# Optimization experiments

Measured on AMD Instinct MI355X. Metric: run time of the kernel, lower is better.

Reference implementation:

```python
import jax, jax.numpy as jnp
import numpy as np

GROUP = 16  # FP4 quantization group size along the K (channel) axis
FP4_MAX = 6.0  # max magnitude representable in e2m1


def _round_e2m1(v):
    """Round to nearest value on the signed e2m1 grid {0,.5,1,1.5,2,3,4,6}."""
    s = jnp.sign(v)
    a = jnp.clip(jnp.abs(v), 0.0, FP4_MAX)
    q = jnp.where(a < 0.25, 0.0,
        jnp.where(a < 0.75, 0.5,
        jnp.where(a < 1.25, 1.0,
        jnp.where(a < 1.75, 1.5,
        jnp.where(a < 2.5, 2.0,
        jnp.where(a < 3.5, 3.0,
        jnp.where(a < 5.0, 4.0, 6.0)))))))
    return s * q


def fake_quant_fp4(x):
    """NVFP4-style fake quantization: per-16 group fp8_e4m3 scale + e2m1 values.

    x: [..., K] with K % 16 == 0. Returns dequantized tensor, same shape/dtype.
    """
    shp = x.shape
    g = x.reshape(shp[:-1] + (shp[-1] // GROUP, GROUP))
    amax = jnp.max(jnp.abs(g), axis=-1, keepdims=True)
    # scale stored as fp8_e4m3 (matches oscales dtype float8_e4m3fn in source)
    scale = (amax / FP4_MAX).astype(jnp.float8_e4m3fn).astype(x.dtype)
    safe = jnp.where(scale > 0, scale, jnp.ones_like(scale))
    q = _round_e2m1(g / safe)
    dq = jnp.where(scale > 0, q * scale, jnp.zeros_like(q))
    return dq.reshape(shp)


def setup_inputs() -> dict:
    key = jax.random.key(0)
    k1, k2, k3 = jax.random.split(key, 3)
    M, K, N = 8192, 4096, 4096
    x = jax.random.normal(k1, (M, K), dtype=jnp.float32)
    weight = jax.random.normal(k2, (N, K), dtype=jnp.float32) * 0.02
    bias = jax.random.normal(k3, (N,), dtype=jnp.float32) * 0.01
    return {"x": x, "weight": weight, "bias": bias}


def reference(x, weight, bias):
    # quantize_input: per-group FP4 fake-quant of activations (smooth == ones)
    xq = fake_quant_fp4(x)
    # __init__ quantizes weight_pad with the same kernel -> qweight/wscales
    wq = fake_quant_fp4(weight)
    # gemm_w4a4 with inline dequant + bias add
    out = jnp.einsum("mk,nk->mn", xq, wq) + bias
    return out
```

## Files before the change

kernel.cpp:

```cpp
#include <hip/hip_runtime.h>
#include <cstdint>


typedef __attribute__((ext_vector_type(8))) __bf16 bf16x8;
typedef __attribute__((ext_vector_type(16))) float f32x16;

typedef __attribute__((address_space(1))) void gvoid;
typedef __attribute__((address_space(3))) void lvoid;

__device__ __forceinline__ float fp8_e4m3_rt(float x) {
    if (x < 0.015625f) {
        return __builtin_rintf(x * 512.0f) * (1.0f / 512.0f);
    }
    unsigned u = __float_as_uint(x);
    unsigned lsb = (u >> 20) & 1u;
    u = (u + 0x7FFFFu + lsb) & ~0xFFFFFu;
    return __uint_as_float(u);
}

__device__ __forceinline__ uint2 quant_quad(float4 v) {
    float ax = fabsf(v.x), ay = fabsf(v.y), az = fabsf(v.z), aw = fabsf(v.w);
    float a = fmaxf(fmaxf(ax, ay), fmaxf(az, aw));
    a = fmaxf(a, __shfl_xor(a, 1));
    a = fmaxf(a, __shfl_xor(a, 2));
    float scale = fp8_e4m3_rt(a / 6.0f);
    float sN = -scale;
    float n0 = sN * 0x1p-27f;
    float n1 = sN * 0x1p-25f;
    float n2 = sN * 0x1p-24f;
    float n4 = sN * 0x1p-23f;
    float n6 = sN * 0x1p-22f;
    float e[4] = {v.x, v.y, v.z, v.w};
    unsigned r[4];
    #pragma unroll
    for (int i = 0; i < 4; ++i) {
        float av = fabsf(e[i]);
        float q =
            fmaf(sN, 0.25f, av) < n0 ? 0.0f :
            fmaf(sN, 0.75f, av) < n1 ? 0.5f :
            fmaf(sN, 1.25f, av) < n2 ? 1.0f :
            fmaf(sN, 1.75f, av) < n2 ? 1.5f :
            fmaf(sN, 2.5f,  av) < n4 ? 2.0f :
            fmaf(sN, 3.5f,  av) < n4 ? 3.0f :
            fmaf(sN, 5.0f,  av) < n6 ? 4.0f : 6.0f;
        float dq = q * scale;
        r[i] = (__float_as_uint(dq) | (__float_as_uint(e[i]) & 0x80000000u)) >> 16;
    }
    uint2 o;
    o.x = r[0] | (r[1] << 16);
    o.y = r[2] | (r[3] << 16);
    return o;
}

__global__ __launch_bounds__(256)
void quant_fp4_fused(const float* __restrict__ x, const float* __restrict__ w,
                     uint16_t* __restrict__ out, int xquads, int totquads) {
    const int half = totquads >> 1;
    const int t0 = blockIdx.x * 256 + threadIdx.x;
    uint2* o2 = (uint2*)out;
    if (t0 < half) {
        const float4* s0 = (t0 < xquads) ? ((const float4*)x) + t0
                                         : ((const float4*)w) + (t0 - xquads);
        o2[t0] = quant_quad(*s0);
    }
    const int q1 = t0 + half;
    if (q1 < totquads) {
        const float4* s1 = (q1 < xquads) ? ((const float4*)x) + q1
                                         : ((const float4*)w) + (q1 - xquads);
        o2[q1] = quant_quad(*s1);
    }
}

#define BM 256
#define BN 256
#define BK 64
#define THREADS 512

#define STG_A(bb, i, kk)                                                     \
    __builtin_amdgcn_global_load_lds((gvoid*)(Aq + (size_t)offA[i] + (kk)),  \
        (lvoid*)&lds[bb][0][ldsU + (i) * 4096], 16, 0, 0)
#define STG_B(bb, i, kk)                                                     \
    __builtin_amdgcn_global_load_lds((gvoid*)(Bq + (size_t)offB[i] + (kk)),  \
        (lvoid*)&lds[bb][1][ldsU + (i) * 4096], 16, 0, 0)

__global__ __launch_bounds__(THREADS, 2)
void gemm_w4a4(const uint16_t* __restrict__ Aq, const uint16_t* __restrict__ Bq,
               const float* __restrict__ bias, float* __restrict__ C,
               int M, int N, int K) {
    __shared__ __align__(16) uint16_t lds[2][2][BM * BK];

    const int tid  = threadIdx.x;
    const int wave = tid >> 6;
    const int lane = tid & 63;
    const int wm   = wave >> 2;
    const int wn   = wave & 3;
    const int l31  = lane & 31;
    const int hi8  = (lane >> 5) << 3;
    const int rsw  = (lane & 7) << 3;

    int kx[4];
    #pragma unroll
    for (int ks = 0; ks < 4; ++ks) kx[ks] = (ks * 16 + hi8) ^ rsw;

    const int aRow = ((wm << 7) + l31) << 6;
    const int bRow = ((wn << 6) + l31) << 6;
    const int ldsU = wave << 9;

    const int ntm = M >> 8, ntn = N >> 8, nwg = ntm * ntn;
    const int bid = blockIdx.x;
    const int q8 = nwg >> 3, r8 = nwg & 7;
    const int xcd = bid & 7;
    const int wgid = (xcd < r8 ? xcd * (q8 + 1) : r8 * (q8 + 1) + (xcd - r8) * q8)
                     + (bid >> 3);
    const int mBase = (wgid % ntm) << 8;
    const int nBase = (wgid / ntm) << 8;
    (void)ntn;

    uint32_t offA[4], offB[4];
    #pragma unroll
    for (int i = 0; i < 4; ++i) {
        const int c   = i * THREADS + tid;
        const int row = c >> 3;
        const int kc  = ((c & 7) ^ (row & 7)) << 3;
        offA[i] = (uint32_t)(mBase + row) * (uint32_t)K + (uint32_t)kc;
        offB[i] = (uint32_t)(nBase + row) * (uint32_t)K + (uint32_t)kc;
    }

    const int nt = K / BK;

    #pragma unroll
    for (int i = 0; i < 4; ++i) STG_A(0, i, 0);
    #pragma unroll
    for (int i = 0; i < 4; ++i) STG_B(0, i, 0);

    f32x16 acc[4][2] = {};

    for (int tk = 0; tk < nt; ++tk) {
        const int bb = tk & 1;
        const uint16_t* lA = &lds[bb][0][0];
        const uint16_t* lB = &lds[bb][1][0];

        asm volatile("" ::: "memory");
        __builtin_amdgcn_s_barrier();
        asm volatile("" ::: "memory");

        if (tk + 1 < nt) {
            const int kk = (tk + 1) * BK;
            #pragma unroll
            for (int i = 0; i < 4; ++i) STG_A(bb ^ 1, i, kk);
            #pragma unroll
            for (int i = 0; i < 4; ++i) STG_B(bb ^ 1, i, kk);
            asm volatile("s_waitcnt vmcnt(8)" ::: "memory");
        } else {
            asm volatile("s_waitcnt vmcnt(0)" ::: "memory");
        }
        __builtin_amdgcn_s_barrier();
        asm volatile("" ::: "memory");

        bf16x8 aC[4], bC[2], aN[4], bN[2];
        #pragma unroll
        for (int mi = 0; mi < 4; ++mi)
            aC[mi] = *(const bf16x8*)&lA[aRow + mi * 2048 + kx[0]];
        #pragma unroll
        for (int ni = 0; ni < 2; ++ni)
            bC[ni] = *(const bf16x8*)&lB[bRow + ni * 2048 + kx[0]];

        #pragma unroll
        for (int ks = 0; ks < 4; ++ks) {
            if (ks < 3) {
                #pragma unroll
                for (int mi = 0; mi < 4; ++mi)
                    aN[mi] = *(const bf16x8*)&lA[aRow + mi * 2048 + kx[ks + 1]];
                #pragma unroll
                for (int ni = 0; ni < 2; ++ni)
                    bN[ni] = *(const bf16x8*)&lB[bRow + ni * 2048 + kx[ks + 1]];
            }
            __builtin_amdgcn_s_setprio(1);
            #pragma unroll
            for (int mi = 0; mi < 4; ++mi)
                #pragma unroll
                for (int ni = 0; ni < 2; ++ni)
                    acc[mi][ni] = __builtin_amdgcn_mfma_f32_32x32x16_bf16(
                        aC[mi], bC[ni], acc[mi][ni], 0, 0, 0);
            __builtin_amdgcn_s_setprio(0);
            if (ks < 3) {
                #pragma unroll
                for (int mi = 0; mi < 4; ++mi) aC[mi] = aN[mi];
                #pragma unroll
                for (int ni = 0; ni < 2; ++ni) bC[ni] = bN[ni];
            }
        }
    }

    #pragma unroll
    for (int ni = 0; ni < 2; ++ni) {
        const int col = nBase + (wn << 6) + ni * 32 + l31;
        const float bj = bias[col];
        #pragma unroll
        for (int mi = 0; mi < 4; ++mi) {
            const int rowb = mBase + (wm << 7) + mi * 32 + ((lane >> 5) << 2);
            #pragma unroll
            for (int r = 0; r < 16; ++r) {
                const int row = rowb + (r & 3) + ((r >> 2) << 3);
                C[(size_t)row * N + col] = acc[mi][ni][r] + bj;
            }
        }
    }
}

extern "C" void kernel_launch(void* const* d_in, const int* in_sizes, int n_in,
                              void* d_out, int out_size, void* d_ws, size_t ws_size,
                              hipStream_t stream) {
    const float* x    = (const float*)d_in[0];
    const float* w    = (const float*)d_in[1];
    const float* bias = (const float*)d_in[2];
    float* out = (float*)d_out;

    const int N = in_sizes[2];
    const int K = in_sizes[1] / N;
    const int M = in_sizes[0] / K;

    uint16_t* xq = (uint16_t*)d_ws;
    uint16_t* wq = xq + (size_t)M * K;
    (void)wq;

    const int xquads = (M * K) / 4;
    const int totquads = xquads + (N * K) / 4;
    const int half = totquads / 2;
    quant_fp4_fused<<<(half + 255) / 256, 256, 0, stream>>>(x, w, xq, xquads, totquads);

    const int nwg = (M >> 8) * (N >> 8);
    gemm_w4a4<<<nwg, THREADS, 0, stream>>>(xq, wq, bias, out, M, N, K);
}
```

Before: 520.8 us.

## Restructure GEMM mainloop into four-phase pipelined schedule with 16x16x32 MFMA

After: 702.5 us. 1.35x slower.

```diff
diff --git a/kernel.cpp b/kernel.cpp
--- a/kernel.cpp
+++ b/kernel.cpp
@@ -3,7 +3,7 @@
 
 
 typedef __attribute__((ext_vector_type(8))) __bf16 bf16x8;
-typedef __attribute__((ext_vector_type(16))) float f32x16;
+typedef __attribute__((ext_vector_type(4))) float f32x4;
 
 typedef __attribute__((address_space(1))) void gvoid;
 typedef __attribute__((address_space(3))) void lvoid;
@@ -71,42 +71,104 @@
     }
 }
 
-#define BM 256
-#define BN 256
 #define BK 64
 #define THREADS 512
 
-#define STG_A(bb, i, kk)                                                     \
-    __builtin_amdgcn_global_load_lds((gvoid*)(Aq + (size_t)offA[i] + (kk)),  \
-        (lvoid*)&lds[bb][0][ldsU + (i) * 4096], 16, 0, 0)
-#define STG_B(bb, i, kk)                                                     \
-    __builtin_amdgcn_global_load_lds((gvoid*)(Bq + (size_t)offB[i] + (kk)),  \
-        (lvoid*)&lds[bb][1][ldsU + (i) * 4096], 16, 0, 0)
+#define SB __builtin_amdgcn_sched_barrier(0)
+
+#define LDA(dst, B_, mh) do { _Pragma("unroll")                               \
+    for (int fi_ = 0; fi_ < 4; ++fi_) {                                       \
+        dst[fi_][0] = *(const bf16x8*)&lds[B_][0][aRowA + (mh)*4096 + fi_*1024 + kx0]; \
+        dst[fi_][1] = *(const bf16x8*)&lds[B_][0][aRowA + (mh)*4096 + fi_*1024 + kx1]; \
+    } } while (0)
+
+#define LDB(dst, B_, nh) do { _Pragma("unroll")                               \
+    for (int fj_ = 0; fj_ < 2; ++fj_) {                                       \
+        dst[fj_][0] = *(const bf16x8*)&lds[B_][1][bRowB + (nh)*8192 + fj_*1024 + kx0]; \
+        dst[fj_][1] = *(const bf16x8*)&lds[B_][1][bRowB + (nh)*8192 + fj_*1024 + kx1]; \
+    } } while (0)
+
+#define STGA(B_, ch, ko) __builtin_amdgcn_global_load_lds(                    \
+    (gvoid*)(pA + offA[ch] + kAdv + (ko)),                                    \
+    (lvoid*)&lds[B_][0][(ch)*4096 + ldsU], 16, 0, 0)
+#define STGB(B_, ch, ko) __builtin_amdgcn_global_load_lds(                    \
+    (gvoid*)(pB + offB[ch] + kAdv + (ko)),                                    \
+    (lvoid*)&lds[B_][1][(ch)*4096 + ldsU], 16, 0, 0)
+
+#define QUAD(A_, Bf_, mh, nh) do {                                            \
+    __builtin_amdgcn_s_setprio(1);                                            \
+    _Pragma("unroll") for (int fi_ = 0; fi_ < 4; ++fi_)                       \
+    _Pragma("unroll") for (int fj_ = 0; fj_ < 2; ++fj_) {                     \
+        f32x4 c_ = acc[(mh)*4 + fi_][(nh)*2 + fj_];                           \
+        c_ = __builtin_amdgcn_mfma_f32_16x16x32_bf16(A_[fi_][0], Bf_[fj_][0], c_, 0, 0, 0); \
+        c_ = __builtin_amdgcn_mfma_f32_16x16x32_bf16(A_[fi_][1], Bf_[fj_][1], c_, 0, 0, 0); \
+        acc[(mh)*4 + fi_][(nh)*2 + fj_] = c_;                                 \
+    }                                                                         \
+    __builtin_amdgcn_s_setprio(0); } while (0)
+
+#define PHEND do { SB; __builtin_amdgcn_s_barrier(); SB; } while (0)
+
+#define KTILE(B_, STG_, AHD_, SK_) do {                                       \
+                                                                     \
+    LDB(b1, B_, 1);                                                           \
+    if (STG_) { STGA(B_, 0, SK_); STGA(B_, 2, SK_); }                         \
+    asm volatile("s_waitcnt lgkmcnt(4)" ::: "memory");                        \
+    if (STG_) { asm volatile("s_waitcnt vmcnt(10)" ::: "memory"); }           \
+    else      { asm volatile("s_waitcnt vmcnt(0)"  ::: "memory"); }           \
+    SB; __builtin_amdgcn_s_barrier(); SB;                                     \
+    QUAD(a0, b0, 0, 0);                                                       \
+    PHEND;                                                                    \
+                                                                     \
+    LDA(a1, B_, 1);                                                           \
+    if (STG_) { STGB(B_, 0, SK_); STGB(B_, 1, SK_); }                         \
+    asm volatile("s_waitcnt lgkmcnt(8)" ::: "memory");                        \
+    if (STG_) { asm volatile("s_waitcnt vmcnt(10)" ::: "memory"); }           \
+    SB; __builtin_amdgcn_s_barrier(); SB;                                     \
+    QUAD(a0, b1, 0, 1);                                                       \
+    PHEND;                                                                    \
+                                                                     \
+    if (AHD_) { LDA(a0, (B_) ^ 1, 0); }                                       \
+    if (STG_) { STGB(B_, 2, SK_); STGB(B_, 3, SK_); }                         \
+    if (AHD_) { asm volatile("s_waitcnt lgkmcnt(8)" ::: "memory"); }          \
+    else      { asm volatile("s_waitcnt lgkmcnt(0)" ::: "memory"); }          \
+    if (STG_) { asm volatile("s_waitcnt vmcnt(10)" ::: "memory"); }           \
+    SB; __builtin_amdgcn_s_barrier(); SB;                                     \
+    QUAD(a1, b1, 1, 1);                                                       \
+    PHEND;                                                                    \
+                                                                     \
+    if (AHD_) { LDB(nb0, (B_) ^ 1, 0); }                                      \
+    if (STG_) { STGA(B_, 1, SK_); STGA(B_, 3, SK_); }                         \
+    if (AHD_) { asm volatile("s_waitcnt lgkmcnt(4)" ::: "memory"); }          \
+    else      { asm volatile("s_waitcnt lgkmcnt(0)" ::: "memory"); }          \
+    if (STG_) { asm volatile("s_waitcnt vmcnt(10)" ::: "memory"); }           \
+    SB; __builtin_amdgcn_s_barrier(); SB;                                     \
+    QUAD(a1, b0, 1, 0);                                                       \
+    if (AHD_) { _Pragma("unroll") for (int z_ = 0; z_ < 2; ++z_) {            \
+        b0[z_][0] = nb0[z_][0]; b0[z_][1] = nb0[z_][1]; } }                   \
+    PHEND;                                                                    \
+    } while (0)
 
 __global__ __launch_bounds__(THREADS, 2)
 void gemm_w4a4(const uint16_t* __restrict__ Aq, const uint16_t* __restrict__ Bq,
                const float* __restrict__ bias, float* __restrict__ C,
                int M, int N, int K) {
-    __shared__ __align__(16) uint16_t lds[2][2][BM * BK];
+    __shared__ __align__(16) uint16_t lds[2][2][256 * BK];
 
     const int tid  = threadIdx.x;
     const int wave = tid >> 6;
     const int lane = tid & 63;
     const int wm   = wave >> 2;
     const int wn   = wave & 3;
-    const int l31  = lane & 31;
-    const int hi8  = (lane >> 5) << 3;
+    const int l15  = lane & 15;
+    const int hi16 = (lane >> 4) << 3;
     const int rsw  = (lane & 7) << 3;
-
-    int kx[4];
-    #pragma unroll
-    for (int ks = 0; ks < 4; ++ks) kx[ks] = (ks * 16 + hi8) ^ rsw;
-
-    const int aRow = ((wm << 7) + l31) << 6;
-    const int bRow = ((wn << 6) + l31) << 6;
-    const int ldsU = wave << 9;
-
-    const int ntm = M >> 8, ntn = N >> 8, nwg = ntm * ntn;
+    const int kx0  = hi16 ^ rsw;
+    const int kx1  = (32 + hi16) ^ rsw;
+    const int aRowA = ((wm << 7) + l15) << 6;
+    const int bRowB = ((wn << 5) + l15) << 6;
+    const int ldsU  = wave << 9;
+
+    const int ntm = M >> 8, nwg = ntm * (N >> 8);
     const int bid = blockIdx.x;
     const int q8 = nwg >> 3, r8 = nwg & 7;
     const int xcd = bid & 7;
@@ -114,96 +176,59 @@
                      + (bid >> 3);
     const int mBase = (wgid % ntm) << 8;
     const int nBase = (wgid / ntm) << 8;
-    (void)ntn;
 
     uint32_t offA[4], offB[4];
     #pragma unroll
     for (int i = 0; i < 4; ++i) {
-        const int c   = i * THREADS + tid;
-        const int row = c >> 3;
-        const int kc  = ((c & 7) ^ (row & 7)) << 3;
-        offA[i] = (uint32_t)(mBase + row) * (uint32_t)K + (uint32_t)kc;
-        offB[i] = (uint32_t)(nBase + row) * (uint32_t)K + (uint32_t)kc;
-    }
+        const int c = i * THREADS + tid;
+        const int p = c >> 3;
+        const int kc = ((c & 7) ^ (p & 7)) << 3;
+        offA[i] = (uint32_t)p * (uint32_t)K + (uint32_t)kc;
+        const int nh = p >> 7, wnn = (p >> 5) & 3, r = p & 31;
+        const int Lr = wnn * 64 + nh * 32 + r;
+        offB[i] = (uint32_t)Lr * (uint32_t)K + (uint32_t)kc;
+    }
+    const uint16_t* pA = Aq + (size_t)mBase * K;
+    const uint16_t* pB = Bq + (size_t)nBase * K;
 
     const int nt = K / BK;
 
+    uint32_t kAdv = 0;
+
+    STGA(0, 0, 0); STGA(0, 2, 0); STGB(0, 0, 0); STGB(0, 1, 0);
+    STGB(0, 2, 0); STGB(0, 3, 0); STGA(0, 1, 0); STGA(0, 3, 0);
+    STGA(1, 0, 64); STGA(1, 2, 64); STGB(1, 0, 64); STGB(1, 1, 64);
+    STGB(1, 2, 64); STGB(1, 3, 64); STGA(1, 1, 64); STGA(1, 3, 64);
+    asm volatile("s_waitcnt vmcnt(8)" ::: "memory");
+    SB; __builtin_amdgcn_s_barrier(); SB;
+
+    f32x4 acc[8][4] = {};
+    bf16x8 a0[4][2], a1[4][2], b0[2][2], b1[2][2], nb0[2][2];
+
+    LDA(a0, 0, 0);
+    LDB(b0, 0, 0);
+
+    kAdv = 2 * BK;
+
+    for (int tk = 0; tk < nt - 2; tk += 2) {
+        KTILE(0, 1, 1, 0);
+        KTILE(1, 1, 1, 64);
+        kAdv += 2 * BK;
+    }
+    KTILE(0, 0, 1, 0);
+    KTILE(1, 0, 0, 0);
+
+    const int rq = (lane >> 4) << 2;
     #pragma unroll
-    for (int i = 0; i < 4; ++i) STG_A(0, i, 0);
-    #pragma unroll
-    for (int i = 0; i < 4; ++i) STG_B(0, i, 0);
-
-    f32x16 acc[4][2] = {};
-
-    for (int tk = 0; tk < nt; ++tk) {
-        const int bb = tk & 1;
-        const uint16_t* lA = &lds[bb][0][0];
-        const uint16_t* lB = &lds[bb][1][0];
-
-        asm volatile("" ::: "memory");
-        __builtin_amdgcn_s_barrier();
-        asm volatile("" ::: "memory");
-
-        if (tk + 1 < nt) {
-            const int kk = (tk + 1) * BK;
-            #pragma unroll
-            for (int i = 0; i < 4; ++i) STG_A(bb ^ 1, i, kk);
-            #pragma unroll
-            for (int i = 0; i < 4; ++i) STG_B(bb ^ 1, i, kk);
-            asm volatile("s_waitcnt vmcnt(8)" ::: "memory");
-        } else {
-            asm volatile("s_waitcnt vmcnt(0)" ::: "memory");
-        }
-        __builtin_amdgcn_s_barrier();
-        asm volatile("" ::: "memory");
-
-        bf16x8 aC[4], bC[2], aN[4], bN[2];
-        #pragma unroll
-        for (int mi = 0; mi < 4; ++mi)
-            aC[mi] = *(const bf16x8*)&lA[aRow + mi * 2048 + kx[0]];
-        #pragma unroll
-        for (int ni = 0; ni < 2; ++ni)
-            bC[ni] = *(const bf16x8*)&lB[bRow + ni * 2048 + kx[0]];
-
-        #pragma unroll
-        for (int ks = 0; ks < 4; ++ks) {
-            if (ks < 3) {
-                #pragma unroll
-                for (int mi = 0; mi < 4; ++mi)
-                    aN[mi] = *(const bf16x8*)&lA[aRow + mi * 2048 + kx[ks + 1]];
-                #pragma unroll
-                for (int ni = 0; ni < 2; ++ni)
-                    bN[ni] = *(const bf16x8*)&lB[bRow + ni * 2048 + kx[ks + 1]];
-            }
-            __builtin_amdgcn_s_setprio(1);
-            #pragma unroll
-            for (int mi = 0; mi < 4; ++mi)
-                #pragma unroll
-                for (int ni = 0; ni < 2; ++ni)
-                    acc[mi][ni] = __builtin_amdgcn_mfma_f32_32x32x16_bf16(
-                        aC[mi], bC[ni], acc[mi][ni], 0, 0, 0);
-            __builtin_amdgcn_s_setprio(0);
-            if (ks < 3) {
-                #pragma unroll
-                for (int mi = 0; mi < 4; ++mi) aC[mi] = aN[mi];
-                #pragma unroll
-                for (int ni = 0; ni < 2; ++ni) bC[ni] = bN[ni];
-            }
-        }
-    }
-
-    #pragma unroll
-    for (int ni = 0; ni < 2; ++ni) {
-        const int col = nBase + (wn << 6) + ni * 32 + l31;
+    for (int j = 0; j < 4; ++j) {
+        const int col = nBase + (wn << 6) + j * 16 + l15;
         const float bj = bias[col];
         #pragma unroll
-        for (int mi = 0; mi < 4; ++mi) {
-            const int rowb = mBase + (wm << 7) + mi * 32 + ((lane >> 5) << 2);
+        for (int i = 0; i < 8; ++i) {
+            const int row0 = mBase + (wm << 7) + i * 16 + rq;
             #pragma unroll
-            for (int r = 0; r < 16; ++r) {
-                const int row = rowb + (r & 3) + ((r >> 2) << 3);
-                C[(size_t)row * N + col] = acc[mi][ni][r] + bj;
-            }
+            for (int r = 0; r < 4; ++r)
+                C[(size_t)(row0 + r) * N + col] = acc[i][j][r] + bj;
         }
     }
 }
@@ -222,7 +247,6 @@
 
     uint16_t* xq = (uint16_t*)d_ws;
     uint16_t* wq = xq + (size_t)M * K;
-    (void)wq;
 
     const int xquads = (M * K) / 4;
     const int totquads = xquads + (N * K) / 4;
```
